# Kernel optimization log

Hardware: AMD Instinct MI355X
Metric: run time of the kernel (lower is better)

Reference implementation:

```python
import jax, jax.numpy as jnp
import numpy as np

N_NODES = 50000
N_EDGES = 800000
IN_DIM = 128
OUT_DIM = 64


def setup_inputs() -> dict:
    key = jax.random.key(0)
    k_x, k_r, k_c, k_v, k_w = jax.random.split(key, 5)
    x = jax.random.normal(k_x, (N_NODES, IN_DIM), dtype=jnp.float32)
    edge_row = jax.random.randint(k_r, (N_EDGES,), 0, N_NODES, dtype=jnp.int64)
    edge_col = jax.random.randint(k_c, (N_EDGES,), 0, N_NODES, dtype=jnp.int64)
    edge_val = jax.random.uniform(k_v, (N_EDGES,), dtype=jnp.float32)
    # kaiming_uniform-style init: bound = sqrt(6 / fan_in) with a=sqrt(5) gain folded in torch;
    # exact init values don't affect correctness testing, use a uniform of similar scale.
    bound = float(np.sqrt(6.0 / IN_DIM))
    weight = jax.random.uniform(k_w, (IN_DIM, OUT_DIM), dtype=jnp.float32,
                                minval=-bound, maxval=bound)
    return {"x": x, "edge_row": edge_row, "edge_col": edge_col,
            "edge_val": edge_val, "weight": weight}


def reference(x, edge_row, edge_col, edge_val, weight):
    # dropout p=0.0 -> identity (module default)
    support = x @ weight                              # [N, out_dim] dense GEMM
    # spmm(adj, support): out[i] = sum_e adj_val[e] * support[col[e]] for row[e]==i
    messages = edge_val[:, None] * support[edge_col]  # [E, out_dim] gather
    out = jax.ops.segment_sum(messages, edge_row, num_segments=N_NODES)  # scatter-add
    return jax.nn.relu(out)
```

## Files before the change

kernel.cpp:

```cpp
#include <hip/hip_runtime.h>

#define N_NODES 50000
#define N_EDGES 800000
#define IN_DIM 128
#define OUT_DIM 64

#define GROUP_SHIFT 6
#define GROUP_ROWS 64
#define N_GROUPS 782
#define SLAB 1216
#define CHUNK2 2048
#define FILL3_BLOCKS 391

typedef _Float16 h4 __attribute__((ext_vector_type(4)));
typedef _Float16 h8 __attribute__((ext_vector_type(8)));
typedef float    f4 __attribute__((ext_vector_type(4)));

#define LDK 136

__global__ __launch_bounds__(256) void gemm_mfma(const float* __restrict__ x,
                                                 const float* __restrict__ w,
                                                 _Float16* __restrict__ support,
                                                 int* __restrict__ gcursor) {
    __shared__ _Float16 xb[GROUP_ROWS * LDK];
    __shared__ _Float16 wt[OUT_DIM * LDK];
    const int tid = threadIdx.x;

    if (tid == 0) gcursor[blockIdx.x] = 0;

    for (int i = tid; i < IN_DIM * OUT_DIM; i += 256) {
        int k = i >> 6, n = i & 63;
        wt[n * LDK + k] = (_Float16)w[i];
    }
    const int rowbase = blockIdx.x * GROUP_ROWS;
    for (int i = tid; i < GROUP_ROWS * (IN_DIM / 4); i += 256) {
        int r  = i >> 5;
        int kq = i & 31;
        int row = rowbase + r;
        float4 v = (row < N_NODES) ? *(const float4*)&x[(size_t)row * IN_DIM + kq * 4]
                                   : make_float4(0.f, 0.f, 0.f, 0.f);
        h4 hv = { (_Float16)v.x, (_Float16)v.y, (_Float16)v.z, (_Float16)v.w };
        *(h4*)&xb[r * LDK + kq * 4] = hv;
    }
    __syncthreads();

    const int wave = tid >> 6;
    const int lane = tid & 63;
    const int mrow = lane & 15;
    const int quad = lane >> 4;
    const int m0   = wave * 16;

    f4 acc[4];
    #pragma unroll
    for (int t = 0; t < 4; ++t) acc[t] = (f4){0.f, 0.f, 0.f, 0.f};

    #pragma unroll
    for (int ks = 0; ks < 4; ++ks) {
        int kof = ks * 32 + quad * 8;
        h8 a = *(h8*)&xb[(m0 + mrow) * LDK + kof];
        #pragma unroll
        for (int t = 0; t < 4; ++t) {
            h8 b = *(h8*)&wt[(t * 16 + mrow) * LDK + kof];
            acc[t] = __builtin_amdgcn_mfma_f32_16x16x32_f16(a, b, acc[t], 0, 0, 0);
        }
    }

    #pragma unroll
    for (int t = 0; t < 4; ++t) {
        #pragma unroll
        for (int r = 0; r < 4; ++r) {
            int row = rowbase + m0 + quad * 4 + r;
            if (row < N_NODES)
                support[(size_t)row * OUT_DIM + t * 16 + mrow] = (_Float16)acc[t][r];
        }
    }
}

__global__ __launch_bounds__(256) void fill3_kernel(const int* __restrict__ erow,
                                                    const int* __restrict__ ecol,
                                                    const float* __restrict__ eval,
                                                    int* __restrict__ gcursor,
                                                    int2* __restrict__ bucket) {
    __shared__ int lcnt[N_GROUPS];
    __shared__ int lbase[N_GROUPS];
    for (int i = threadIdx.x; i < N_GROUPS; i += 256) lcnt[i] = 0;
    __syncthreads();
    const int base = blockIdx.x * CHUNK2;
    #pragma unroll 4
    for (int i = 0; i < CHUNK2 / 256; ++i) {
        int e = base + threadIdx.x + i * 256;
        if (e < N_EDGES) atomicAdd(&lcnt[erow[e] >> GROUP_SHIFT], 1);
    }
    __syncthreads();
    for (int i = threadIdx.x; i < N_GROUPS; i += 256) {
        int c = lcnt[i];
        lbase[i] = c ? atomicAdd(&gcursor[i], c) : 0;
        lcnt[i]  = 0;
    }
    __syncthreads();
    #pragma unroll 4
    for (int i = 0; i < CHUNK2 / 256; ++i) {
        int e = base + threadIdx.x + i * 256;
        if (e < N_EDGES) {
            int r = erow[e];
            int g = r >> GROUP_SHIFT;
            int p = atomicAdd(&lcnt[g], 1);
            bucket[(size_t)g * SLAB + lbase[g] + p] =
                make_int2(((r & (GROUP_ROWS - 1)) << 16) | ecol[e],
                          __float_as_int(eval[e]));
        }
    }
}

__global__ __launch_bounds__(256) void group_reduce(const int* __restrict__ gcursor,
                                                    const int2* __restrict__ bucket,
                                                    const _Float16* __restrict__ support,
                                                    float* __restrict__ out) {
    __shared__ int2 ebuf[SLAB];
    __shared__ int2 ebuf2[SLAB];
    __shared__ int  rcnt[GROUP_ROWS];
    __shared__ int  rstart[GROUP_ROWS + 1];
    __shared__ int  rcur[GROUP_ROWS];
    const int grp = blockIdx.x;
    const int cnt = gcursor[grp];
    const long long start = (long long)grp * SLAB;
    const int tid = threadIdx.x;

    if (tid < GROUP_ROWS) rcnt[tid] = 0;
    __syncthreads();
    for (int j = tid; j < cnt; j += 256) {
        int2 cv = bucket[start + j];
        ebuf[j] = cv;
        atomicAdd(&rcnt[cv.x >> 16], 1);
    }
    __syncthreads();
    if (tid < GROUP_ROWS) {
        int v = rcnt[tid];
        int s = v;
        #pragma unroll
        for (int off = 1; off < 64; off <<= 1) {
            int t = __shfl_up(s, off, 64);
            if (tid >= off) s += t;
        }
        int excl = s - v;
        rstart[tid] = excl;
        rcur[tid]   = excl;
        if (tid == 63) rstart[64] = s;
    }
    __syncthreads();
    for (int j = tid; j < cnt; j += 256) {
        int2 cv = ebuf[j];
        int rl = cv.x >> 16;
        int p  = atomicAdd(&rcur[rl], 1);
        ebuf2[p] = cv;
    }
    __syncthreads();

    const int g     = tid & 15;
    const int local = tid >> 4;
    const int rowbase = grp * GROUP_ROWS;
    #pragma unroll
    for (int rr = 0; rr < 4; ++rr) {
        const int rl  = local + rr * 16;
        const int row = rowbase + rl;
        const int jb  = rstart[rl];
        const int je  = rstart[rl + 1];
        float4 acc = make_float4(0.f, 0.f, 0.f, 0.f);
        for (int j = jb; j < je; ++j) {
            int2 cv = ebuf2[j];
            int col = cv.x & 0xFFFF;
            float v = __int_as_float(cv.y);
            h4 sr = *(const h4*)&support[(size_t)col * OUT_DIM + g * 4];
            acc.x += v * (float)sr[0];
            acc.y += v * (float)sr[1];
            acc.z += v * (float)sr[2];
            acc.w += v * (float)sr[3];
        }
        if (row < N_NODES) {
            acc.x = fmaxf(acc.x, 0.f);
            acc.y = fmaxf(acc.y, 0.f);
            acc.z = fmaxf(acc.z, 0.f);
            acc.w = fmaxf(acc.w, 0.f);
            *(float4*)&out[(size_t)row * OUT_DIM + g * 4] = acc;
        }
    }
}

extern "C" void kernel_launch(void* const* d_in, const int* in_sizes, int n_in,
                              void* d_out, int out_size, void* d_ws, size_t ws_size,
                              hipStream_t stream) {
    const float* x    = (const float*)d_in[0];
    const int*   erow = (const int*)  d_in[1];
    const int*   ecol = (const int*)  d_in[2];
    const float* ev   = (const float*)d_in[3];
    const float* w    = (const float*)d_in[4];
    float* out = (float*)d_out;

    char* ws = (char*)d_ws;
    _Float16* support = (_Float16*)ws;
    int*  gcursor = (int*)(ws + 6400000);
    int2* bucket  = (int2*)(ws + 6403200);

    gemm_mfma<<<N_GROUPS, 256, 0, stream>>>(x, w, support, gcursor);
    fill3_kernel<<<FILL3_BLOCKS, 256, 0, stream>>>(erow, ecol, ev, gcursor, bucket);
    group_reduce<<<N_GROUPS, 256, 0, stream>>>(gcursor, bucket, support, out);
}
```

Before: 146.1 us.

## Fuse GEMM and bucket fill into one launch, split reduce into 16-row blocks

```diff
diff --git a/kernel.cpp b/kernel.cpp
--- a/kernel.cpp
+++ b/kernel.cpp
@@ -10,7 +10,10 @@
 #define N_GROUPS 782
 #define SLAB 1216
 #define CHUNK2 2048
-#define FILL3_BLOCKS 391
+#define FILL_BLOCKS 391
+
+#define RPB 16
+#define EB_CAP 448
 
 typedef _Float16 h4 __attribute__((ext_vector_type(4)));
 typedef _Float16 h8 __attribute__((ext_vector_type(8)));
@@ -18,171 +21,167 @@
 
 #define LDK 136
 
-__global__ __launch_bounds__(256) void gemm_mfma(const float* __restrict__ x,
-                                                 const float* __restrict__ w,
-                                                 _Float16* __restrict__ support,
-                                                 int* __restrict__ gcursor) {
-    __shared__ _Float16 xb[GROUP_ROWS * LDK];
-    __shared__ _Float16 wt[OUT_DIM * LDK];
+__global__ __launch_bounds__(256) void fused_gemm_fill(const float* __restrict__ x,
+                                                       const float* __restrict__ w,
+                                                       const int* __restrict__ erow,
+                                                       const int* __restrict__ ecol,
+                                                       const float* __restrict__ eval,
+                                                       _Float16* __restrict__ support,
+                                                       int* __restrict__ gcursor,
+                                                       int2* __restrict__ bucket) {
+    __shared__ char smem[GROUP_ROWS * LDK * 2 + OUT_DIM * LDK * 2];
     const int tid = threadIdx.x;
 
-    if (tid == 0) gcursor[blockIdx.x] = 0;
-
-    for (int i = tid; i < IN_DIM * OUT_DIM; i += 256) {
-        int k = i >> 6, n = i & 63;
-        wt[n * LDK + k] = (_Float16)w[i];
-    }
-    const int rowbase = blockIdx.x * GROUP_ROWS;
-    for (int i = tid; i < GROUP_ROWS * (IN_DIM / 4); i += 256) {
-        int r  = i >> 5;
-        int kq = i & 31;
-        int row = rowbase + r;
-        float4 v = (row < N_NODES) ? *(const float4*)&x[(size_t)row * IN_DIM + kq * 4]
-                                   : make_float4(0.f, 0.f, 0.f, 0.f);
-        h4 hv = { (_Float16)v.x, (_Float16)v.y, (_Float16)v.z, (_Float16)v.w };
-        *(h4*)&xb[r * LDK + kq * 4] = hv;
-    }
-    __syncthreads();
-
-    const int wave = tid >> 6;
-    const int lane = tid & 63;
-    const int mrow = lane & 15;
-    const int quad = lane >> 4;
-    const int m0   = wave * 16;
-
-    f4 acc[4];
-    #pragma unroll
-    for (int t = 0; t < 4; ++t) acc[t] = (f4){0.f, 0.f, 0.f, 0.f};
-
-    #pragma unroll
-    for (int ks = 0; ks < 4; ++ks) {
-        int kof = ks * 32 + quad * 8;
-        h8 a = *(h8*)&xb[(m0 + mrow) * LDK + kof];
+    if (blockIdx.x < N_GROUPS) {
+        _Float16* xb = (_Float16*)smem;
+        _Float16* wt = (_Float16*)(smem + GROUP_ROWS * LDK * 2);
+
+        for (int i = tid; i < IN_DIM * OUT_DIM; i += 256) {
+            int k = i >> 6, n = i & 63;
+            wt[n * LDK + k] = (_Float16)w[i];
+        }
+        const int rowbase = blockIdx.x * GROUP_ROWS;
+        for (int i = tid; i < GROUP_ROWS * (IN_DIM / 4); i += 256) {
+            int r  = i >> 5;
+            int kq = i & 31;
+            int row = rowbase + r;
+            float4 v = (row < N_NODES)
+                           ? *(const float4*)&x[(size_t)row * IN_DIM + kq * 4]
+                           : make_float4(0.f, 0.f, 0.f, 0.f);
+            h4 hv = { (_Float16)v.x, (_Float16)v.y, (_Float16)v.z, (_Float16)v.w };
+            *(h4*)&xb[r * LDK + kq * 4] = hv;
+        }
+        __syncthreads();
+
+        const int wave = tid >> 6;
+        const int lane = tid & 63;
+        const int mrow = lane & 15;
+        const int quad = lane >> 4;
+        const int m0   = wave * 16;
+
+        f4 acc[4];
+        #pragma unroll
+        for (int t = 0; t < 4; ++t) acc[t] = (f4){0.f, 0.f, 0.f, 0.f};
+
+        #pragma unroll
+        for (int ks = 0; ks < 4; ++ks) {
+            int kof = ks * 32 + quad * 8;
+            h8 a = *(h8*)&xb[(m0 + mrow) * LDK + kof];
+            #pragma unroll
+            for (int t = 0; t < 4; ++t) {
+                h8 b = *(h8*)&wt[(t * 16 + mrow) * LDK + kof];
+                acc[t] = __builtin_amdgcn_mfma_f32_16x16x32_f16(a, b, acc[t], 0, 0, 0);
+            }
+        }
+
         #pragma unroll
         for (int t = 0; t < 4; ++t) {
-            h8 b = *(h8*)&wt[(t * 16 + mrow) * LDK + kof];
-            acc[t] = __builtin_amdgcn_mfma_f32_16x16x32_f16(a, b, acc[t], 0, 0, 0);
-        }
-    }
-
-    #pragma unroll
-    for (int t = 0; t < 4; ++t) {
-        #pragma unroll
-        for (int r = 0; r < 4; ++r) {
-            int row = rowbase + m0 + quad * 4 + r;
-            if (row < N_NODES)
-                support[(size_t)row * OUT_DIM + t * 16 + mrow] = (_Float16)acc[t][r];
+            #pragma unroll
+            for (int r = 0; r < 4; ++r) {
+                int row = rowbase + m0 + quad * 4 + r;
+                if (row < N_NODES)
+                    support[(size_t)row * OUT_DIM + t * 16 + mrow] = (_Float16)acc[t][r];
+            }
+        }
+    } else {
+        int* lcnt  = (int*)smem;
+        int* lbase = lcnt + N_GROUPS;
+        for (int i = tid; i < N_GROUPS; i += 256) lcnt[i] = 0;
+        __syncthreads();
+        const int base = (blockIdx.x - N_GROUPS) * CHUNK2;
+        #pragma unroll 4
+        for (int i = 0; i < CHUNK2 / 256; ++i) {
+            int e = base + tid + i * 256;
+            if (e < N_EDGES) atomicAdd(&lcnt[erow[e] >> GROUP_SHIFT], 1);
+        }
+        __syncthreads();
+        for (int i = tid; i < N_GROUPS; i += 256) {
+            int c = lcnt[i];
+            lbase[i] = c ? atomicAdd(&gcursor[i], c) : 0;
+            lcnt[i]  = 0;
+        }
+        __syncthreads();
+        #pragma unroll 4
+        for (int i = 0; i < CHUNK2 / 256; ++i) {
+            int e = base + tid + i * 256;
+            if (e < N_EDGES) {
+                int r = erow[e];
+                int g = r >> GROUP_SHIFT;
+                int p = atomicAdd(&lcnt[g], 1);
+                bucket[(size_t)g * SLAB + lbase[g] + p] =
+                    make_int2(((r & (GROUP_ROWS - 1)) << 16) | ecol[e],
+                              __float_as_int(eval[e]));
+            }
         }
     }
 }
 
-__global__ __launch_bounds__(256) void fill3_kernel(const int* __restrict__ erow,
-                                                    const int* __restrict__ ecol,
-                                                    const float* __restrict__ eval,
-                                                    int* __restrict__ gcursor,
-                                                    int2* __restrict__ bucket) {
-    __shared__ int lcnt[N_GROUPS];
-    __shared__ int lbase[N_GROUPS];
-    for (int i = threadIdx.x; i < N_GROUPS; i += 256) lcnt[i] = 0;
-    __syncthreads();
-    const int base = blockIdx.x * CHUNK2;
-    #pragma unroll 4
-    for (int i = 0; i < CHUNK2 / 256; ++i) {
-        int e = base + threadIdx.x + i * 256;
-        if (e < N_EDGES) atomicAdd(&lcnt[erow[e] >> GROUP_SHIFT], 1);
-    }
-    __syncthreads();
-    for (int i = threadIdx.x; i < N_GROUPS; i += 256) {
-        int c = lcnt[i];
-        lbase[i] = c ? atomicAdd(&gcursor[i], c) : 0;
-        lcnt[i]  = 0;
-    }
-    __syncthreads();
-    #pragma unroll 4
-    for (int i = 0; i < CHUNK2 / 256; ++i) {
-        int e = base + threadIdx.x + i * 256;
-        if (e < N_EDGES) {
-            int r = erow[e];
-            int g = r >> GROUP_SHIFT;
-            int p = atomicAdd(&lcnt[g], 1);
-            bucket[(size_t)g * SLAB + lbase[g] + p] =
-                make_int2(((r & (GROUP_ROWS - 1)) << 16) | ecol[e],
-                          __float_as_int(eval[e]));
-        }
-    }
-}
-
-__global__ __launch_bounds__(256) void group_reduce(const int* __restrict__ gcursor,
-                                                    const int2* __restrict__ bucket,
-                                                    const _Float16* __restrict__ support,
-                                                    float* __restrict__ out) {
-    __shared__ int2 ebuf[SLAB];
-    __shared__ int2 ebuf2[SLAB];
-    __shared__ int  rcnt[GROUP_ROWS];
-    __shared__ int  rstart[GROUP_ROWS + 1];
-    __shared__ int  rcur[GROUP_ROWS];
-    const int grp = blockIdx.x;
-    const int cnt = gcursor[grp];
-    const long long start = (long long)grp * SLAB;
+__global__ __launch_bounds__(256) void reduce16(const int* __restrict__ gcursor,
+                                                const int2* __restrict__ bucket,
+                                                const _Float16* __restrict__ support,
+                                                float* __restrict__ out) {
+    __shared__ int2 ebuf[EB_CAP];
+    __shared__ int  rcnt[RPB];
+    __shared__ int  rstart[RPB + 1];
+    __shared__ int  rcur[RPB];
+    const int grp = blockIdx.x >> 2;
+    const int sub = blockIdx.x & 3;
+    const int cnt = min(gcursor[grp], SLAB);
+    const size_t sb = (size_t)grp * SLAB;
     const int tid = threadIdx.x;
 
-    if (tid < GROUP_ROWS) rcnt[tid] = 0;
+    if (tid < RPB) rcnt[tid] = 0;
     __syncthreads();
     for (int j = tid; j < cnt; j += 256) {
-        int2 cv = bucket[start + j];
-        ebuf[j] = cv;
-        atomicAdd(&rcnt[cv.x >> 16], 1);
-    }
-    __syncthreads();
-    if (tid < GROUP_ROWS) {
+        int rl = bucket[sb + j].x >> 16;
+        if ((rl >> 4) == sub) atomicAdd(&rcnt[rl & 15], 1);
+    }
+    __syncthreads();
+    if (tid < RPB) {
         int v = rcnt[tid];
         int s = v;
         #pragma unroll
-        for (int off = 1; off < 64; off <<= 1) {
+        for (int off = 1; off < RPB; off <<= 1) {
             int t = __shfl_up(s, off, 64);
             if (tid >= off) s += t;
         }
-        int excl = s - v;
-        rstart[tid] = excl;
-        rcur[tid]   = excl;
-        if (tid == 63) rstart[64] = s;
+        rstart[tid] = s - v;
+        rcur[tid]   = s - v;
+        if (tid == RPB - 1) rstart[RPB] = s;
     }
     __syncthreads();
     for (int j = tid; j < cnt; j += 256) {
+        int2 cv = bucket[sb + j];
+        int rl = cv.x >> 16;
+        if ((rl >> 4) == sub) {
+            int p = atomicAdd(&rcur[rl & 15], 1);
+            if (p < EB_CAP) ebuf[p] = cv;
+        }
+    }
+    __syncthreads();
+
+    const int g  = tid & 15;
+    const int lr = tid >> 4;
+    const int row = grp * GROUP_ROWS + sub * RPB + lr;
+    const int jb = rstart[lr];
+    const int je = min(rstart[lr + 1], EB_CAP);
+    float4 acc = make_float4(0.f, 0.f, 0.f, 0.f);
+    for (int j = jb; j < je; ++j) {
         int2 cv = ebuf[j];
-        int rl = cv.x >> 16;
-        int p  = atomicAdd(&rcur[rl], 1);
-        ebuf2[p] = cv;
-    }
-    __syncthreads();
-
-    const int g     = tid & 15;
-    const int local = tid >> 4;
-    const int rowbase = grp * GROUP_ROWS;
-    #pragma unroll
-    for (int rr = 0; rr < 4; ++rr) {
-        const int rl  = local + rr * 16;
-        const int row = rowbase + rl;
-        const int jb  = rstart[rl];
-        const int je  = rstart[rl + 1];
-        float4 acc = make_float4(0.f, 0.f, 0.f, 0.f);
-        for (int j = jb; j < je; ++j) {
-            int2 cv = ebuf2[j];
-            int col = cv.x & 0xFFFF;
-            float v = __int_as_float(cv.y);
-            h4 sr = *(const h4*)&support[(size_t)col * OUT_DIM + g * 4];
-            acc.x += v * (float)sr[0];
-            acc.y += v * (float)sr[1];
-            acc.z += v * (float)sr[2];
-            acc.w += v * (float)sr[3];
-        }
-        if (row < N_NODES) {
-            acc.x = fmaxf(acc.x, 0.f);
-            acc.y = fmaxf(acc.y, 0.f);
-            acc.z = fmaxf(acc.z, 0.f);
-            acc.w = fmaxf(acc.w, 0.f);
-            *(float4*)&out[(size_t)row * OUT_DIM + g * 4] = acc;
-        }
+        int col = cv.x & 0xFFFF;
+        float v = __int_as_float(cv.y);
+        h4 sr = *(const h4*)&support[(size_t)col * OUT_DIM + g * 4];
+        acc.x += v * (float)sr[0];
+        acc.y += v * (float)sr[1];
+        acc.z += v * (float)sr[2];
+        acc.w += v * (float)sr[3];
+    }
+    if (row < N_NODES) {
+        acc.x = fmaxf(acc.x, 0.f);
+        acc.y = fmaxf(acc.y, 0.f);
+        acc.z = fmaxf(acc.z, 0.f);
+        acc.w = fmaxf(acc.w, 0.f);
+        *(float4*)&out[(size_t)row * OUT_DIM + g * 4] = acc;
     }
 }
 
@@ -201,7 +200,10 @@
     int*  gcursor = (int*)(ws + 6400000);
     int2* bucket  = (int2*)(ws + 6403200);
 
-    gemm_mfma<<<N_GROUPS, 256, 0, stream>>>(x, w, support, gcursor);
-    fill3_kernel<<<FILL3_BLOCKS, 256, 0, stream>>>(erow, ecol, ev, gcursor, bucket);
-    group_reduce<<<N_GROUPS, 256, 0, stream>>>(gcursor, bucket, support, out);
+    hipMemsetAsync(gcursor, 0, sizeof(int) * N_GROUPS, stream);
+
+    fused_gemm_fill<<<N_GROUPS + FILL_BLOCKS, 256, 0, stream>>>(
+        x, w, erow, ecol, ev, support, gcursor, bucket);
+
+    reduce16<<<N_GROUPS * 4, 256, 0, stream>>>(gcursor, bucket, support, out);
 }
```

New measurement: 131.9 us. 9.7% less time.
